# Kernel tuning notes

Hardware: AMD Instinct MI355X
Metric: run time of the kernel (lower is better)

The kernel has to match this reference:

```python
import jax, jax.numpy as jnp
import numpy as np

TEMPERATURE = 8.0  # sqrt(d_head=64)
MASK_FILL = -1e9


def setup_inputs() -> dict:
    key = jax.random.key(0)
    kq, kk, kv, km = jax.random.split(key, 4)
    B, H, L, D = 4, 16, 2048, 64
    return {
        "query": jax.random.normal(kq, (B, H, L, D), dtype=jnp.float32),
        "key": jax.random.normal(kk, (B, H, L, D), dtype=jnp.float32),
        "value": jax.random.normal(kv, (B, H, L, D), dtype=jnp.float32),
        "mask": jax.random.randint(km, (B, 1, L, L), 0, 2, dtype=jnp.int32),
    }


def reference(query, key, value, mask):
    # scores: [B, H, Lq, Lk]
    scores = jnp.einsum("bhqd,bhkd->bhqk", query / TEMPERATURE, key)
    scores = jnp.where(mask == 0, MASK_FILL, scores)
    # sigmoid attention (no row normalization); dropout omitted (eval mode)
    attn = jax.nn.sigmoid(scores)
    output = jnp.einsum("bhqk,bhkd->bhqd", attn, value)
    return (output, attn)
```

## Files before the change

kernel.cpp:

```cpp
#include <hip/hip_runtime.h>
#include <hip/hip_bf16.h>
#include <stdint.h>

#define B_ 4
#define H_ 16
#define L_ 2048
#define D_ 64
#define BH (B_ * H_)

typedef __attribute__((ext_vector_type(8))) short short8;
typedef __attribute__((ext_vector_type(4))) float f32x4;

__device__ __forceinline__ short b16(float f) {
  __hip_bfloat16 h = __float2bfloat16(f);
  return __builtin_bit_cast(short, h);
}

__global__ __launch_bounds__(256) void vt_kernel(const float* __restrict__ V,
                                                 unsigned short* __restrict__ Vt) {
  __shared__ unsigned short lds[64 * 68];
  int bid = blockIdx.x;
  int bh  = bid >> 5;
  int kt  = bid & 31;
  int t   = threadIdx.x;
  const float* vsrc = V + ((size_t)bh * L_ + (size_t)kt * 64) * D_;
#pragma unroll
  for (int i = 0; i < 4; ++i) {
    int f4  = i * 256 + t;
    int row = f4 >> 4;
    int c4  = (f4 & 15) << 2;
    float4 v = *reinterpret_cast<const float4*>(vsrc + row * D_ + c4);
    ushort4 u;
    u.x = (unsigned short)b16(v.x);
    u.y = (unsigned short)b16(v.y);
    u.z = (unsigned short)b16(v.z);
    u.w = (unsigned short)b16(v.w);
    *reinterpret_cast<ushort4*>(&lds[row * 68 + c4]) = u;
  }
  __syncthreads();
  unsigned short* dst = Vt + (size_t)bh * D_ * L_ + (size_t)kt * 64;
#pragma unroll
  for (int i = 0; i < 8; ++i) {
    int c  = i * 256 + t;
    int d  = c >> 5;
    int k2 = (c & 31) * 2;
    unsigned int lo = lds[(k2 + 0) * 68 + d];
    unsigned int hi = lds[(k2 + 1) * 68 + d];
    *reinterpret_cast<unsigned int*>(dst + d * L_ + k2) = lo | (hi << 16);
  }
}

__global__ __launch_bounds__(256, 4) void attn3_kernel(
    const float* __restrict__ Q, const float* __restrict__ K,
    const int* __restrict__ M, const unsigned short* __restrict__ Vt,
    float* __restrict__ O, float* __restrict__ A) {
  __shared__ unsigned short Kl[64 * 64];
  __shared__ unsigned short Vl[64 * 64];
  __shared__ unsigned short Pl[64 * 64];

  int wg  = blockIdx.x;
  int xcd = wg & 7;
  int j   = wg >> 3;
  int g   = xcd * 16 + (j & 15);
  int b   = g >> 5;
  int qt  = g & 31;
  int h   = j >> 4;
  int bh  = b * 16 + h;

  int t    = threadIdx.x;
  int lane = t & 63;
  int w    = t >> 6;
  int wr   = w >> 1;
  int wc   = w & 1;
  int lr   = lane & 15;
  int lg   = lane >> 4;

  short8 qf[2][2];
  const float* qbase = Q + ((size_t)bh * L_ + (size_t)qt * 64 + wr * 32) * D_;
#pragma unroll
  for (int m = 0; m < 2; ++m) {
#pragma unroll
    for (int ks = 0; ks < 2; ++ks) {
      const float4* p = reinterpret_cast<const float4*>(qbase + (m * 16 + lr) * D_ + ks * 32 + lg * 8);
      float4 a = p[0], c = p[1];
      qf[m][ks] = (short8){b16(a.x * 0.125f), b16(a.y * 0.125f), b16(a.z * 0.125f), b16(a.w * 0.125f),
                           b16(c.x * 0.125f), b16(c.y * 0.125f), b16(c.z * 0.125f), b16(c.w * 0.125f)};
    }
  }

  f32x4 o[2][2] = {};
  const int* mbase = M + (size_t)b * L_ * L_;
  float* abase = A + (size_t)bh * L_ * L_;
  const float* kbase0 = K + (size_t)bh * L_ * D_;
  const unsigned short* vbase0 = Vt + (size_t)bh * D_ * L_;
  int qrow = qt * 64 + wr * 32;

  for (int ki = 0; ki < 32; ++ki) {
    int k0 = ki * 64;

    int4 mv[2][2];
#pragma unroll
    for (int m = 0; m < 2; ++m)
#pragma unroll
      for (int n = 0; n < 2; ++n)
        mv[m][n] = *reinterpret_cast<const int4*>(
            mbase + (size_t)(qrow + m * 16 + lr) * L_ + k0 + wc * 32 + n * 16 + lg * 4);

    __syncthreads();

    const float* ksrc = kbase0 + (size_t)k0 * D_;
#pragma unroll
    for (int i = 0; i < 4; ++i) {
      int f4  = i * 256 + t;
      int row = f4 >> 4;
      int c4  = (f4 & 15) << 2;
      float4 v = *reinterpret_cast<const float4*>(ksrc + row * D_ + c4);
      ushort4 u;
      u.x = (unsigned short)b16(v.x);
      u.y = (unsigned short)b16(v.y);
      u.z = (unsigned short)b16(v.z);
      u.w = (unsigned short)b16(v.w);
      *reinterpret_cast<ushort4*>(&Kl[row * 64 + (c4 ^ ((row & 7) << 3))]) = u;
    }
    const unsigned short* vsrc = vbase0 + k0;
#pragma unroll
    for (int i = 0; i < 2; ++i) {
      int gidx = i * 256 + t;
      int row  = gidx >> 3;
      int c0   = (gidx & 7) << 3;
      uint4 v = *reinterpret_cast<const uint4*>(vsrc + (size_t)row * L_ + c0);
      *reinterpret_cast<uint4*>(&Vl[row * 64 + (c0 ^ ((row & 7) << 3))]) = v;
    }
    __syncthreads();

    f32x4 s[2][2] = {};
#pragma unroll
    for (int ks = 0; ks < 2; ++ks) {
      short8 kf[2];
#pragma unroll
      for (int n = 0; n < 2; ++n) {
        int row = wc * 32 + n * 16 + lr;
        int col = ks * 32 + lg * 8;
        kf[n] = *reinterpret_cast<const short8*>(&Kl[row * 64 + (col ^ ((row & 7) << 3))]);
      }
#pragma unroll
      for (int m = 0; m < 2; ++m)
#pragma unroll
        for (int n = 0; n < 2; ++n)
          s[m][n] = __builtin_amdgcn_mfma_f32_16x16x32_bf16(kf[n], qf[m][ks], s[m][n], 0, 0, 0);
    }

#pragma unroll
    for (int m = 0; m < 2; ++m) {
#pragma unroll
      for (int n = 0; n < 2; ++n) {
        f32x4 f;
        ushort4 u;
#pragma unroll
        for (int r = 0; r < 4; ++r) {
          float sv = s[m][n][r];
          float e  = __builtin_amdgcn_exp2f(sv * -1.44269504f);
          float at = ((&mv[m][n].x)[r] != 0)
                         ? __builtin_amdgcn_rcpf(1.0f + e)
                         : 0.0f;
          f[r] = at;
          (&u.x)[r] = (unsigned short)b16(at);
        }
        __builtin_nontemporal_store(f, reinterpret_cast<f32x4*>(
            abase + (size_t)(qrow + m * 16 + lr) * L_ + k0 + wc * 32 + n * 16 + lg * 4));
        int q  = wr * 32 + m * 16 + lr;
        int kl = wc * 32 + n * 16 + lg * 4;
        *reinterpret_cast<ushort4*>(&Pl[q * 64 + (kl ^ ((q & 7) << 3))]) = u;
      }
    }
    __syncthreads();

#pragma unroll
    for (int ks = 0; ks < 2; ++ks) {
      short8 pf[2], vf[2];
#pragma unroll
      for (int m = 0; m < 2; ++m) {
        int row = wr * 32 + m * 16 + lr;
        int col = ks * 32 + lg * 8;
        pf[m] = *reinterpret_cast<const short8*>(&Pl[row * 64 + (col ^ ((row & 7) << 3))]);
      }
#pragma unroll
      for (int n = 0; n < 2; ++n) {
        int row = wc * 32 + n * 16 + lr;
        int col = ks * 32 + lg * 8;
        vf[n] = *reinterpret_cast<const short8*>(&Vl[row * 64 + (col ^ ((row & 7) << 3))]);
      }
#pragma unroll
      for (int m = 0; m < 2; ++m)
#pragma unroll
        for (int n = 0; n < 2; ++n)
          o[m][n] = __builtin_amdgcn_mfma_f32_16x16x32_bf16(pf[m], vf[n], o[m][n], 0, 0, 0);
    }
  }

  float* obase = O + ((size_t)bh * L_ + (size_t)qt * 64 + wr * 32) * D_;
#pragma unroll
  for (int m = 0; m < 2; ++m)
#pragma unroll
    for (int n = 0; n < 2; ++n)
#pragma unroll
      for (int r = 0; r < 4; ++r)
        __builtin_nontemporal_store(o[m][n][r],
            &obase[(m * 16 + lg * 4 + r) * D_ + wc * 32 + n * 16 + lr]);
}

extern "C" void kernel_launch(void* const* d_in, const int* in_sizes, int n_in,
                              void* d_out, int out_size, void* d_ws, size_t ws_size,
                              hipStream_t stream) {
  (void)in_sizes; (void)n_in; (void)out_size; (void)ws_size;
  const float* Q = (const float*)d_in[0];
  const float* K = (const float*)d_in[1];
  const float* V = (const float*)d_in[2];
  const int*   M = (const int*)d_in[3];
  float* O = (float*)d_out;
  float* A = (float*)d_out + (size_t)BH * L_ * D_;
  unsigned short* Vt = (unsigned short*)d_ws;

  vt_kernel<<<BH * 32, 256, 0, stream>>>(V, Vt);
  attn3_kernel<<<BH * 32, 256, 0, stream>>>(Q, K, M, Vt, O, A);
}
```

Before: 319.6 us.

## Double-buffer K/V tiles in LDS with register prefetch of next tile

Loads the next K and V tiles into registers at the start of each iteration and writes them, converted to bf16, into a second LDS buffer after the PV MFMAs. This hides global load latency behind compute and removes one barrier per iteration. It costs extra LDS (two K/V buffers) and more live registers, which may pressure occupancy under the 4-block launch bound.

```diff
diff --git a/kernel.cpp b/kernel.cpp
--- a/kernel.cpp
+++ b/kernel.cpp
@@ -50,13 +50,13 @@
   }
 }
 
-__global__ __launch_bounds__(256, 4) void attn3_kernel(
+__global__ __launch_bounds__(256, 4) void attn4_kernel(
     const float* __restrict__ Q, const float* __restrict__ K,
     const int* __restrict__ M, const unsigned short* __restrict__ Vt,
     float* __restrict__ O, float* __restrict__ A) {
-  __shared__ unsigned short Kl[64 * 64];
-  __shared__ unsigned short Vl[64 * 64];
-  __shared__ unsigned short Pl[64 * 64];
+  __shared__ unsigned short Kl[2][4096];
+  __shared__ unsigned short Vl[2][4096];
+  __shared__ unsigned short Pl[4096];
 
   int wg  = blockIdx.x;
   int xcd = wg & 7;
@@ -95,8 +95,59 @@
   const unsigned short* vbase0 = Vt + (size_t)bh * D_ * L_;
   int qrow = qt * 64 + wr * 32;
 
+  int krow[4], kc4[4];
+#pragma unroll
+  for (int i = 0; i < 4; ++i) {
+    int f4  = i * 256 + t;
+    krow[i] = f4 >> 4;
+    kc4[i]  = (f4 & 15) << 2;
+  }
+  int vrow[2], vc0[2];
+#pragma unroll
+  for (int i = 0; i < 2; ++i) {
+    int gi  = i * 256 + t;
+    vrow[i] = gi >> 3;
+    vc0[i]  = (gi & 7) << 3;
+  }
+
+  float4 kreg[4];
+  uint4  vreg[2];
+
+#pragma unroll
+  for (int i = 0; i < 4; ++i)
+    kreg[i] = *reinterpret_cast<const float4*>(kbase0 + krow[i] * D_ + kc4[i]);
+#pragma unroll
+  for (int i = 0; i < 2; ++i)
+    vreg[i] = *reinterpret_cast<const uint4*>(vbase0 + (size_t)vrow[i] * L_ + vc0[i]);
+#pragma unroll
+  for (int i = 0; i < 4; ++i) {
+    ushort4 u;
+    u.x = (unsigned short)b16(kreg[i].x);
+    u.y = (unsigned short)b16(kreg[i].y);
+    u.z = (unsigned short)b16(kreg[i].z);
+    u.w = (unsigned short)b16(kreg[i].w);
+    *reinterpret_cast<ushort4*>(&Kl[0][krow[i] * 64 + (kc4[i] ^ ((krow[i] & 7) << 3))]) = u;
+  }
+#pragma unroll
+  for (int i = 0; i < 2; ++i)
+    *reinterpret_cast<uint4*>(&Vl[0][vrow[i] * 64 + (vc0[i] ^ ((vrow[i] & 7) << 3))]) = vreg[i];
+
   for (int ki = 0; ki < 32; ++ki) {
-    int k0 = ki * 64;
+    int cur = ki & 1;
+    int k0  = ki * 64;
+
+    __syncthreads();
+
+    if (ki + 1 < 32) {
+      const float* ksrc = kbase0 + (size_t)(k0 + 64) * D_;
+      const unsigned short* vsrc = vbase0 + k0 + 64;
+#pragma unroll
+      for (int i = 0; i < 4; ++i)
+        kreg[i] = *reinterpret_cast<const float4*>(ksrc + krow[i] * D_ + kc4[i]);
+#pragma unroll
+      for (int i = 0; i < 2; ++i)
+        vreg[i] = *reinterpret_cast<const uint4*>(vsrc + (size_t)vrow[i] * L_ + vc0[i]);
+    }
 
     int4 mv[2][2];
 #pragma unroll
@@ -106,33 +157,6 @@
         mv[m][n] = *reinterpret_cast<const int4*>(
             mbase + (size_t)(qrow + m * 16 + lr) * L_ + k0 + wc * 32 + n * 16 + lg * 4);
 
-    __syncthreads();
-
-    const float* ksrc = kbase0 + (size_t)k0 * D_;
-#pragma unroll
-    for (int i = 0; i < 4; ++i) {
-      int f4  = i * 256 + t;
-      int row = f4 >> 4;
-      int c4  = (f4 & 15) << 2;
-      float4 v = *reinterpret_cast<const float4*>(ksrc + row * D_ + c4);
-      ushort4 u;
-      u.x = (unsigned short)b16(v.x);
-      u.y = (unsigned short)b16(v.y);
-      u.z = (unsigned short)b16(v.z);
-      u.w = (unsigned short)b16(v.w);
-      *reinterpret_cast<ushort4*>(&Kl[row * 64 + (c4 ^ ((row & 7) << 3))]) = u;
-    }
-    const unsigned short* vsrc = vbase0 + k0;
-#pragma unroll
-    for (int i = 0; i < 2; ++i) {
-      int gidx = i * 256 + t;
-      int row  = gidx >> 3;
-      int c0   = (gidx & 7) << 3;
-      uint4 v = *reinterpret_cast<const uint4*>(vsrc + (size_t)row * L_ + c0);
-      *reinterpret_cast<uint4*>(&Vl[row * 64 + (c0 ^ ((row & 7) << 3))]) = v;
-    }
-    __syncthreads();
-
     f32x4 s[2][2] = {};
 #pragma unroll
     for (int ks = 0; ks < 2; ++ks) {
@@ -141,7 +165,7 @@
       for (int n = 0; n < 2; ++n) {
         int row = wc * 32 + n * 16 + lr;
         int col = ks * 32 + lg * 8;
-        kf[n] = *reinterpret_cast<const short8*>(&Kl[row * 64 + (col ^ ((row & 7) << 3))]);
+        kf[n] = *reinterpret_cast<const short8*>(&Kl[cur][row * 64 + (col ^ ((row & 7) << 3))]);
       }
 #pragma unroll
       for (int m = 0; m < 2; ++m)
@@ -188,13 +212,28 @@
       for (int n = 0; n < 2; ++n) {
         int row = wc * 32 + n * 16 + lr;
         int col = ks * 32 + lg * 8;
-        vf[n] = *reinterpret_cast<const short8*>(&Vl[row * 64 + (col ^ ((row & 7) << 3))]);
+        vf[n] = *reinterpret_cast<const short8*>(&Vl[cur][row * 64 + (col ^ ((row & 7) << 3))]);
       }
 #pragma unroll
       for (int m = 0; m < 2; ++m)
 #pragma unroll
         for (int n = 0; n < 2; ++n)
           o[m][n] = __builtin_amdgcn_mfma_f32_16x16x32_bf16(pf[m], vf[n], o[m][n], 0, 0, 0);
+    }
+
+    if (ki + 1 < 32) {
+#pragma unroll
+      for (int i = 0; i < 4; ++i) {
+        ushort4 u;
+        u.x = (unsigned short)b16(kreg[i].x);
+        u.y = (unsigned short)b16(kreg[i].y);
+        u.z = (unsigned short)b16(kreg[i].z);
+        u.w = (unsigned short)b16(kreg[i].w);
+        *reinterpret_cast<ushort4*>(&Kl[cur ^ 1][krow[i] * 64 + (kc4[i] ^ ((krow[i] & 7) << 3))]) = u;
+      }
+#pragma unroll
+      for (int i = 0; i < 2; ++i)
+        *reinterpret_cast<uint4*>(&Vl[cur ^ 1][vrow[i] * 64 + (vc0[i] ^ ((vrow[i] & 7) << 3))]) = vreg[i];
     }
   }
 
@@ -222,5 +261,5 @@
   unsigned short* Vt = (unsigned short*)d_ws;
 
   vt_kernel<<<BH * 32, 256, 0, stream>>>(V, Vt);
-  attn3_kernel<<<BH * 32, 256, 0, stream>>>(Q, K, M, Vt, O, A);
-}
+  attn4_kernel<<<BH * 32, 256, 0, stream>>>(Q, K, M, Vt, O, A);
+}
```

Result: slower. 387.5 us (+21.2%).

## Pre-swizzle K and V to bf16 tiles and double-buffer LDS loads

Applied to the files above, without the earlier changes.

A prep kernel now converts K to bf16 and transposes V into swizzled 64x64 bf16 tiles that can be copied straight into LDS. The attention kernel double-buffers the K and V LDS tiles, prefetching the next tile into registers during compute, and needs one fewer barrier per iteration. This removes repeated fp32 K loads and conversions in every query block and hides global latency. In exchange it adds workspace traffic for the bf16 K copy, more LDS per block (which may lower occupancy), and extra register pressure.

```diff
diff --git a/kernel.cpp b/kernel.cpp
--- a/kernel.cpp
+++ b/kernel.cpp
@@ -7,6 +7,7 @@
 #define L_ 2048
 #define D_ 64
 #define BH (B_ * H_)
+#define NT (BH * 32)
 
 typedef __attribute__((ext_vector_type(8))) short short8;
 typedef __attribute__((ext_vector_type(4))) float f32x4;
@@ -16,47 +17,69 @@
   return __builtin_bit_cast(short, h);
 }
 
-__global__ __launch_bounds__(256) void vt_kernel(const float* __restrict__ V,
-                                                 unsigned short* __restrict__ Vt) {
+__global__ __launch_bounds__(256) void prep_kernel(const float* __restrict__ K,
+                                                   const float* __restrict__ V,
+                                                   unsigned short* __restrict__ Kb,
+                                                   unsigned short* __restrict__ Vb) {
   __shared__ unsigned short lds[64 * 68];
   int bid = blockIdx.x;
-  int bh  = bid >> 5;
-  int kt  = bid & 31;
   int t   = threadIdx.x;
-  const float* vsrc = V + ((size_t)bh * L_ + (size_t)kt * 64) * D_;
-#pragma unroll
-  for (int i = 0; i < 4; ++i) {
-    int f4  = i * 256 + t;
-    int row = f4 >> 4;
-    int c4  = (f4 & 15) << 2;
-    float4 v = *reinterpret_cast<const float4*>(vsrc + row * D_ + c4);
-    ushort4 u;
-    u.x = (unsigned short)b16(v.x);
-    u.y = (unsigned short)b16(v.y);
-    u.z = (unsigned short)b16(v.z);
-    u.w = (unsigned short)b16(v.w);
-    *reinterpret_cast<ushort4*>(&lds[row * 68 + c4]) = u;
+  if (bid < NT) {
+    const float* src = K + (size_t)bid * 64 * D_;
+    unsigned short* dst = Kb + (size_t)bid * 4096;
+#pragma unroll
+    for (int i = 0; i < 4; ++i) {
+      int f4  = i * 256 + t;
+      int row = f4 >> 4;
+      int c4  = (f4 & 15) << 2;
+      float4 v = *reinterpret_cast<const float4*>(src + row * D_ + c4);
+      ushort4 u;
+      u.x = (unsigned short)b16(v.x);
+      u.y = (unsigned short)b16(v.y);
+      u.z = (unsigned short)b16(v.z);
+      u.w = (unsigned short)b16(v.w);
+      *reinterpret_cast<ushort4*>(&dst[row * 64 + (c4 ^ ((row & 7) << 3))]) = u;
+    }
+  } else {
+    bid -= NT;
+    const float* src = V + (size_t)bid * 64 * D_;
+#pragma unroll
+    for (int i = 0; i < 4; ++i) {
+      int f4  = i * 256 + t;
+      int row = f4 >> 4;
+      int c4  = (f4 & 15) << 2;
+      float4 v = *reinterpret_cast<const float4*>(src + row * D_ + c4);
+      ushort4 u;
+      u.x = (unsigned short)b16(v.x);
+      u.y = (unsigned short)b16(v.y);
+      u.z = (unsigned short)b16(v.z);
+      u.w = (unsigned short)b16(v.w);
+      *reinterpret_cast<ushort4*>(&lds[row * 68 + c4]) = u;
+    }
+    __syncthreads();
+    unsigned short* dst = Vb + (size_t)bid * 4096;
+#pragma unroll
+    for (int i = 0; i < 4; ++i) {
+      int g  = i * 256 + t;
+      int r  = g >> 4;
+      int c4 = (g & 15) << 2;
+      ushort4 u;
+      u.x = lds[(c4 + 0) * 68 + r];
+      u.y = lds[(c4 + 1) * 68 + r];
+      u.z = lds[(c4 + 2) * 68 + r];
+      u.w = lds[(c4 + 3) * 68 + r];
+      *reinterpret_cast<ushort4*>(&dst[r * 64 + (c4 ^ ((r & 7) << 3))]) = u;
+    }
   }
-  __syncthreads();
-  unsigned short* dst = Vt + (size_t)bh * D_ * L_ + (size_t)kt * 64;
-#pragma unroll
-  for (int i = 0; i < 8; ++i) {
-    int c  = i * 256 + t;
-    int d  = c >> 5;
-    int k2 = (c & 31) * 2;
-    unsigned int lo = lds[(k2 + 0) * 68 + d];
-    unsigned int hi = lds[(k2 + 1) * 68 + d];
-    *reinterpret_cast<unsigned int*>(dst + d * L_ + k2) = lo | (hi << 16);
-  }
-}
-
-__global__ __launch_bounds__(256, 4) void attn3_kernel(
-    const float* __restrict__ Q, const float* __restrict__ K,
-    const int* __restrict__ M, const unsigned short* __restrict__ Vt,
+}
+
+__global__ __launch_bounds__(256, 4) void attn5_kernel(
+    const float* __restrict__ Q, const int* __restrict__ M,
+    const unsigned short* __restrict__ Kb, const unsigned short* __restrict__ Vb,
     float* __restrict__ O, float* __restrict__ A) {
-  __shared__ unsigned short Kl[64 * 64];
-  __shared__ unsigned short Vl[64 * 64];
-  __shared__ unsigned short Pl[64 * 64];
+  __shared__ __align__(16) unsigned short Kl[2][4096];
+  __shared__ __align__(16) unsigned short Vl[2][4096];
+  __shared__ __align__(16) unsigned short Pl[4096];
 
   int wg  = blockIdx.x;
   int xcd = wg & 7;
@@ -91,12 +114,28 @@
   f32x4 o[2][2] = {};
   const int* mbase = M + (size_t)b * L_ * L_;
   float* abase = A + (size_t)bh * L_ * L_;
-  const float* kbase0 = K + (size_t)bh * L_ * D_;
-  const unsigned short* vbase0 = Vt + (size_t)bh * D_ * L_;
+  const unsigned short* kb = Kb + (size_t)(bh * 32) * 4096;
+  const unsigned short* vb = Vb + (size_t)(bh * 32) * 4096;
   int qrow = qt * 64 + wr * 32;
 
+  int s0 = t * 8;
+  int s1 = t * 8 + 2048;
+
+  uint4 kpre[2], vpre[2];
+
+  kpre[0] = *reinterpret_cast<const uint4*>(kb + s0);
+  kpre[1] = *reinterpret_cast<const uint4*>(kb + s1);
+  vpre[0] = *reinterpret_cast<const uint4*>(vb + s0);
+  vpre[1] = *reinterpret_cast<const uint4*>(vb + s1);
+  *reinterpret_cast<uint4*>(&Kl[0][s0]) = kpre[0];
+  *reinterpret_cast<uint4*>(&Kl[0][s1]) = kpre[1];
+  *reinterpret_cast<uint4*>(&Vl[0][s0]) = vpre[0];
+  *reinterpret_cast<uint4*>(&Vl[0][s1]) = vpre[1];
+  __syncthreads();
+
   for (int ki = 0; ki < 32; ++ki) {
-    int k0 = ki * 64;
+    int cur = ki & 1;
+    int k0  = ki * 64;
 
     int4 mv[2][2];
 #pragma unroll
@@ -106,32 +145,14 @@
         mv[m][n] = *reinterpret_cast<const int4*>(
             mbase + (size_t)(qrow + m * 16 + lr) * L_ + k0 + wc * 32 + n * 16 + lg * 4);
 
-    __syncthreads();
-
-    const float* ksrc = kbase0 + (size_t)k0 * D_;
-#pragma unroll
-    for (int i = 0; i < 4; ++i) {
-      int f4  = i * 256 + t;
-      int row = f4 >> 4;
-      int c4  = (f4 & 15) << 2;
-      float4 v = *reinterpret_cast<const float4*>(ksrc + row * D_ + c4);
-      ushort4 u;
-      u.x = (unsigned short)b16(v.x);
-      u.y = (unsigned short)b16(v.y);
-      u.z = (unsigned short)b16(v.z);
-      u.w = (unsigned short)b16(v.w);
-      *reinterpret_cast<ushort4*>(&Kl[row * 64 + (c4 ^ ((row & 7) << 3))]) = u;
-    }
-    const unsigned short* vsrc = vbase0 + k0;
-#pragma unroll
-    for (int i = 0; i < 2; ++i) {
-      int gidx = i * 256 + t;
-      int row  = gidx >> 3;
-      int c0   = (gidx & 7) << 3;
-      uint4 v = *reinterpret_cast<const uint4*>(vsrc + (size_t)row * L_ + c0);
-      *reinterpret_cast<uint4*>(&Vl[row * 64 + (c0 ^ ((row & 7) << 3))]) = v;
-    }
-    __syncthreads();
+    if (ki + 1 < 32) {
+      const unsigned short* ks_ = kb + (size_t)(ki + 1) * 4096;
+      const unsigned short* vs_ = vb + (size_t)(ki + 1) * 4096;
+      kpre[0] = *reinterpret_cast<const uint4*>(ks_ + s0);
+      kpre[1] = *reinterpret_cast<const uint4*>(ks_ + s1);
+      vpre[0] = *reinterpret_cast<const uint4*>(vs_ + s0);
+      vpre[1] = *reinterpret_cast<const uint4*>(vs_ + s1);
+    }
 
     f32x4 s[2][2] = {};
 #pragma unroll
@@ -141,7 +162,7 @@
       for (int n = 0; n < 2; ++n) {
         int row = wc * 32 + n * 16 + lr;
         int col = ks * 32 + lg * 8;
-        kf[n] = *reinterpret_cast<const short8*>(&Kl[row * 64 + (col ^ ((row & 7) << 3))]);
+        kf[n] = *reinterpret_cast<const short8*>(&Kl[cur][row * 64 + (col ^ ((row & 7) << 3))]);
       }
 #pragma unroll
       for (int m = 0; m < 2; ++m)
@@ -188,7 +209,7 @@
       for (int n = 0; n < 2; ++n) {
         int row = wc * 32 + n * 16 + lr;
         int col = ks * 32 + lg * 8;
-        vf[n] = *reinterpret_cast<const short8*>(&Vl[row * 64 + (col ^ ((row & 7) << 3))]);
+        vf[n] = *reinterpret_cast<const short8*>(&Vl[cur][row * 64 + (col ^ ((row & 7) << 3))]);
       }
 #pragma unroll
       for (int m = 0; m < 2; ++m)
@@ -196,6 +217,14 @@
         for (int n = 0; n < 2; ++n)
           o[m][n] = __builtin_amdgcn_mfma_f32_16x16x32_bf16(pf[m], vf[n], o[m][n], 0, 0, 0);
     }
+
+    if (ki + 1 < 32) {
+      *reinterpret_cast<uint4*>(&Kl[cur ^ 1][s0]) = kpre[0];
+      *reinterpret_cast<uint4*>(&Kl[cur ^ 1][s1]) = kpre[1];
+      *reinterpret_cast<uint4*>(&Vl[cur ^ 1][s0]) = vpre[0];
+      *reinterpret_cast<uint4*>(&Vl[cur ^ 1][s1]) = vpre[1];
+    }
+    __syncthreads();
   }
 
   float* obase = O + ((size_t)bh * L_ + (size_t)qt * 64 + wr * 32) * D_;
@@ -219,8 +248,9 @@
   const int*   M = (const int*)d_in[3];
   float* O = (float*)d_out;
   float* A = (float*)d_out + (size_t)BH * L_ * D_;
-  unsigned short* Vt = (unsigned short*)d_ws;
-
-  vt_kernel<<<BH * 32, 256, 0, stream>>>(V, Vt);
-  attn3_kernel<<<BH * 32, 256, 0, stream>>>(Q, K, M, Vt, O, A);
-}
+  unsigned short* Kb = (unsigned short*)d_ws;
+  unsigned short* Vb = (unsigned short*)d_ws + (size_t)NT * 4096;
+
+  prep_kernel<<<2 * NT, 256, 0, stream>>>(K, V, Kb, Vb);
+  attn5_kernel<<<NT, 256, 0, stream>>>(Q, M, Kb, Vb, O, A);
+}
```

New measurement: 490.9 us. +53.6%, slower.
